# Kernel optimization log

Measured on AMD Instinct MI355X. Metric: run time of the kernel, lower is better.

The kernel has to match this reference:

```python
import jax, jax.numpy as jnp
import numpy as np

B, S, D, F, E, K, H = 4, 1024, 512, 2048, 8, 2, 8
HEAD_DIM = D // H


def setup_inputs() -> dict:
    key = jax.random.key(0)
    ks = jax.random.split(key, 8)
    s = 0.02
    return {
        "x": jax.random.normal(ks[0], (B, S, D), jnp.float32),
        "gate_Wk": jax.random.normal(ks[1], (D, D), jnp.float32) * s,
        "gate_bk": jnp.zeros((D,), jnp.float32),
        "expert_queries": jax.random.normal(ks[2], (E, D), jnp.float32),
        "Wqkv": jax.random.normal(ks[3], (E, 3 * D, D), jnp.float32) * s,
        "bqkv": jnp.zeros((E, 3 * D), jnp.float32),
        "Wo": jax.random.normal(ks[4], (E, D, D), jnp.float32) * s,
        "bo": jnp.zeros((E, D), jnp.float32),
        "g1": jnp.ones((E, D), jnp.float32),
        "be1": jnp.zeros((E, D), jnp.float32),
        "W1": jax.random.normal(ks[5], (E, F, D), jnp.float32) * s,
        "bf1": jnp.zeros((E, F), jnp.float32),
        "W2": jax.random.normal(ks[6], (E, D, F), jnp.float32) * s,
        "bf2": jnp.zeros((E, D), jnp.float32),
        "g2": jnp.ones((E, D), jnp.float32),
        "be2": jnp.zeros((E, D), jnp.float32),
    }


def _layernorm(x, g, b):
    m = x.mean(-1, keepdims=True)
    v = ((x - m) ** 2).mean(-1, keepdims=True)
    return (x - m) * jax.lax.rsqrt(v + 1e-5) * g + b


def _expert(x, Wqkv, bqkv, Wo, bo, g1, be1, W1, bf1, W2, bf2, g2, be2):
    # x: [B,S,D]; one ExpertTransformerDecoder block (dropout=0, eval)
    b, s, d = x.shape
    qkv = x @ Wqkv.T + bqkv                      # [B,S,3D]
    q, k, v = jnp.split(qkv, 3, axis=-1)
    to_heads = lambda t: t.reshape(b, s, H, HEAD_DIM).transpose(0, 2, 1, 3)
    q, k, v = to_heads(q), to_heads(k), to_heads(v)
    scale = 1.0 / np.sqrt(HEAD_DIM).astype(np.float32)
    attn = jax.nn.softmax(jnp.einsum('bhqd,bhkd->bhqk', q * scale, k), axis=-1)
    ctx = jnp.einsum('bhqk,bhkd->bhqd', attn, v).transpose(0, 2, 1, 3).reshape(b, s, d)
    ctx = ctx @ Wo.T + bo
    x = _layernorm(x + ctx, g1, be1)
    h = jax.nn.gelu(x @ W1.T + bf1, approximate=False)
    h = jax.nn.gelu(h @ W2.T + bf2, approximate=False)
    return _layernorm(x + h, g2, be2)


def reference(x, gate_Wk, gate_bk, expert_queries, Wqkv, bqkv, Wo, bo,
              g1, be1, W1, bf1, W2, bf2, g2, be2):
    # attention gating: softmax over experts of <key_proj(x), expert_q> * d^-0.5
    keys = x @ gate_Wk.T + gate_bk                      # [B,S,D]
    scores = jnp.einsum('bsd,ed->bse', keys, expert_queries) * (D ** -0.5)
    probs = jax.nn.softmax(scores, axis=-1)             # [B,S,E]
    # top-k mask + renormalize
    _, idx = jax.lax.top_k(probs, K)                    # [B,S,K]
    mask = jax.nn.one_hot(idx, E, dtype=probs.dtype).sum(-2)
    gated = probs * mask
    gated = gated / (gated.sum(-1, keepdims=True) + 1e-9)
    # run all experts densely (as the torch code does), vmapped over E
    eo = jax.vmap(_expert, in_axes=(None,) + (0,) * 12)(
        x, Wqkv, bqkv, Wo, bo, g1, be1, W1, bf1, W2, bf2, g2, be2)  # [E,B,S,D]
    return jnp.einsum('ebsd,bse->bsd', eo, gated)
```

## Files before the change

### kernel.cpp

```cpp
#include <hip/hip_runtime.h>
#include <cstdint>
#include <cmath>

#define Bc 4
#define Sc 1024
#define Dc 512
#define Fc 2048
#define Ec 8
#define Hc 8
#define Mc 4096

typedef unsigned short u16;
typedef __attribute__((ext_vector_type(8))) short bf16x8;
typedef __attribute__((ext_vector_type(4))) float f32x4;

__device__ __forceinline__ float bf2f(u16 u) {
  unsigned v = ((unsigned)u) << 16;
  return __builtin_bit_cast(float, v);
}
__device__ __forceinline__ u16 f2bf(float f) {
  unsigned u = __builtin_bit_cast(unsigned, f);
  unsigned r = 0x7fffu + ((u >> 16) & 1u);
  return (u16)((u + r) >> 16);
}
__device__ __forceinline__ unsigned pack2bf(float a, float b) {
  return (unsigned)f2bf(a) | ((unsigned)f2bf(b) << 16);
}
__device__ __forceinline__ float gelu_f(float x) {
  const float z = 1.5957691216057308f * fmaf(0.044715f * x, x * x, x);
  const float e = __expf(z);
  return x * (1.0f - __builtin_amdgcn_rcpf(e + 1.0f));
}
__device__ __forceinline__ void async16(const void* g, void* l) {
  __builtin_amdgcn_global_load_lds(
      (const __attribute__((address_space(1))) unsigned int*)g,
      (__attribute__((address_space(3))) unsigned int*)l, 16, 0, 0);
}

__global__ __launch_bounds__(256) void cvt_kernel(const float* __restrict__ in,
                                                  u16* __restrict__ outp, long long n) {
  const long long i = ((long long)blockIdx.x * 256 + threadIdx.x) * 4;
  if (i < n) {
    const float4 v = *(const float4*)(in + i);
    ushort4 o;
    o.x = f2bf(v.x); o.y = f2bf(v.y); o.z = f2bf(v.z); o.w = f2bf(v.w);
    *(ushort4*)(outp + i) = o;
  }
}

__global__ __launch_bounds__(256) void weq_kernel(const float* __restrict__ gWk,
                                                  const float* __restrict__ eq,
                                                  float* __restrict__ weq) {
  __shared__ float red[4][64];
  const int tid = threadIdx.x, wave = tid >> 6, lane = tid & 63;
  const int d = blockIdx.x * 64 + lane;
  const int e = blockIdx.y;
  float acc = 0.f;
  for (int j = wave * 128; j < wave * 128 + 128; ++j)
    acc += gWk[(long long)j * 512 + d] * eq[e * 512 + j];
  red[wave][lane] = acc;
  __syncthreads();
  if (wave == 0)
    weq[e * 512 + d] = red[0][lane] + red[1][lane] + red[2][lane] + red[3][lane];
}
__global__ void beq_kernel(const float* __restrict__ gbk, const float* __restrict__ eq,
                           float* __restrict__ beq) {
  const int wave = threadIdx.x >> 6, lane = threadIdx.x & 63;
  for (int e = wave; e < 8; e += 4) {
    float a = 0.f;
#pragma unroll
    for (int i = 0; i < 8; ++i) a += gbk[lane + 64 * i] * eq[e * 512 + lane + 64 * i];
#pragma unroll
    for (int off = 32; off; off >>= 1) a += __shfl_xor(a, off);
    if (lane == 0) beq[e] = a;
  }
}

__global__ __launch_bounds__(256) void gate_kernel(const float* __restrict__ x,
                                                   const float* __restrict__ weq,
                                                   const float* __restrict__ beq,
                                                   float* __restrict__ gated,
                                                   int* __restrict__ cnt, int* __restrict__ tlist,
                                                   int* __restrict__ pos) {
  const int wave = threadIdx.x >> 6, lane = threadIdx.x & 63;
  const int t = blockIdx.x * 4 + wave;
  const float* xr = x + (long long)t * 512;
  float acc[8] = {};
#pragma unroll
  for (int i = 0; i < 8; ++i) {
    const float xv = xr[lane + 64 * i];
#pragma unroll
    for (int e2 = 0; e2 < 8; ++e2) acc[e2] += xv * weq[e2 * 512 + lane + 64 * i];
  }
#pragma unroll
  for (int e2 = 0; e2 < 8; ++e2)
#pragma unroll
    for (int off = 32; off; off >>= 1) acc[e2] += __shfl_xor(acc[e2], off);
  if (lane == 0) {
    const float scale = 0.044194173824159216f;
    float s[8], mx = -1e30f;
#pragma unroll
    for (int e2 = 0; e2 < 8; ++e2) { s[e2] = (acc[e2] + beq[e2]) * scale; mx = fmaxf(mx, s[e2]); }
    float p[8], sum = 0.f;
#pragma unroll
    for (int e2 = 0; e2 < 8; ++e2) { p[e2] = expf(s[e2] - mx); sum += p[e2]; }
#pragma unroll
    for (int e2 = 0; e2 < 8; ++e2) p[e2] /= sum;
    int i1 = 0;
#pragma unroll
    for (int e2 = 1; e2 < 8; ++e2) if (p[e2] > p[i1]) i1 = e2;
    int i2 = (i1 == 0) ? 1 : 0;
#pragma unroll
    for (int e2 = 0; e2 < 8; ++e2) if (e2 != i1 && e2 != i2 && p[e2] > p[i2]) i2 = e2;
    const float denom = p[i1] + p[i2] + 1e-9f;
#pragma unroll
    for (int e2 = 0; e2 < 8; ++e2)
      gated[t * 8 + e2] = (e2 == i1 || e2 == i2) ? p[e2] / denom : 0.f;
    const int b = t >> 10;
    int s1 = atomicAdd(cnt + i1 * 4 + b, 1);
    tlist[(i1 * 4 + b) * 1024 + s1] = t;
    pos[i1 * 4096 + t] = s1;
    int s2 = atomicAdd(cnt + i2 * 4 + b, 1);
    tlist[(i2 * 4 + b) * 1024 + s2] = t;
    pos[i2 * 4096 + t] = s2;
  }
}

__global__ void pad_kernel(const int* __restrict__ cnt, int* __restrict__ tlist) {
  const int seg = blockIdx.x;
  const int c = cnt[seg];
  const int ce = (c + 127) & ~127;
  const int tpad = (seg & 3) << 10;
  for (int i = c + (int)threadIdx.x; i < ce; i += 128) tlist[seg * 1024 + i] = tpad;
}

__global__ void wl_kernel(const int* __restrict__ cnt, int* __restrict__ wl) {
  const int seg = threadIdx.x;
  if (seg >= 32) return;
  int base = 0;
  for (int s = 0; s < seg; ++s) base += (cnt[s] + 127) >> 7;
  const int nt = (cnt[seg] + 127) >> 7;
  for (int t = 0; t < nt; ++t) wl[base + t] = (seg << 8) | t;
  if (seg == 31) wl[96] = base + nt;
}

template <int GELU, int QKV, int ROUTED, int BK>
__global__ __launch_bounds__(256) void gemm_bf16(
    const u16* __restrict__ A, const u16* __restrict__ Bw, const float* __restrict__ bias,
    u16* __restrict__ Cout, u16* __restrict__ vT, int M, int N, int K, long long Astride,
    const int* __restrict__ wl) {
  int e;
  long long bm;
  if (ROUTED) {
    const int total = wl[96];
    if ((int)blockIdx.x >= total) return;
    const int item = wl[blockIdx.x];
    const int seg = item >> 8, tile = item & 255;
    e = seg >> 2;
    bm = ((long long)(seg & 3) << 10) + tile * 128;
  } else {
    e = blockIdx.z;
    bm = (long long)blockIdx.x * 128;
  }
  __shared__ __attribute__((aligned(16))) u16 As[128 * BK];
  __shared__ __attribute__((aligned(16))) u16 Bs[128 * BK];
  const int tid = threadIdx.x;
  const int wave = tid >> 6, lane = tid & 63;
  const long long bn = (long long)blockIdx.y * 128;
  const u16* Ag = A + (long long)e * Astride + bm * K;
  const u16* Bg = Bw + ((long long)e * N + bn) * K;
  constexpr int LPR = BK / 8;
  constexpr int RPI = 512 / BK;
  constexpr int IPW = BK / 16;
  const int lrow = lane / LPR, lpos = lane % LPR;
  const int lm = lane & 15, quad = lane >> 4;
  const int wm = (wave >> 1) * 64, wn = (wave & 1) * 64;
  f32x4 acc[4][4] = {};
  for (int kk = 0; kk < K; kk += BK) {
    __syncthreads();
#pragma unroll
    for (int i = 0; i < IPW; ++i) {
      const int gi = wave * IPW + i;
      const int row = gi * RPI + lrow;
      const int sc = lpos ^ (row & 7);
      async16(Ag + (long long)row * K + kk + sc * 8, &As[gi * 512]);
      async16(Bg + (long long)row * K + kk + sc * 8, &Bs[gi * 512]);
    }
    __syncthreads();
#pragma unroll
    for (int ks = 0; ks < BK / 32; ++ks) {
      bf16x8 af[4], bfr[4];
#pragma unroll
      for (int mi = 0; mi < 4; ++mi) {
        const int row = wm + mi * 16 + lm;
        const int ch = (ks * 4 + quad) ^ (row & 7);
        af[mi] = *(const bf16x8*)(As + row * BK + ch * 8);
      }
#pragma unroll
      for (int nj = 0; nj < 4; ++nj) {
        const int row = wn + nj * 16 + lm;
        const int ch = (ks * 4 + quad) ^ (row & 7);
        bfr[nj] = *(const bf16x8*)(Bs + row * BK + ch * 8);
      }
#pragma unroll
      for (int mi = 0; mi < 4; ++mi)
#pragma unroll
        for (int nj = 0; nj < 4; ++nj)
          acc[mi][nj] = __builtin_amdgcn_mfma_f32_16x16x32_bf16(bfr[nj], af[mi], acc[mi][nj], 0, 0, 0);
    }
  }
  const float* bs = bias + (long long)e * N;
#pragma unroll
  for (int mi = 0; mi < 4; ++mi) {
    const int m = (int)bm + wm + mi * 16 + lm;
#pragma unroll
    for (int nj = 0; nj < 4; ++nj) {
      const int n0 = (int)bn + wn + nj * 16 + quad * 4;
      const float4 bv = *(const float4*)(bs + n0);
      float v0 = acc[mi][nj][0] + bv.x;
      float v1 = acc[mi][nj][1] + bv.y;
      float v2 = acc[mi][nj][2] + bv.z;
      float v3 = acc[mi][nj][3] + bv.w;
      if (GELU) { v0 = gelu_f(v0); v1 = gelu_f(v1); v2 = gelu_f(v2); v3 = gelu_f(v3); }
      if (QKV) {
        if (n0 < 1024) {
          uint2 pk; pk.x = pack2bf(v0, v1); pk.y = pack2bf(v2, v3);
          *(uint2*)(Cout + ((long long)e * Mc + m) * 1024 + n0) = pk;
        } else {
          const int hh = (n0 - 1024) >> 6, dd = (n0 - 1024) & 63;
          const int bb = m >> 10, ss = m & 1023;
          u16* vp = vT + ((((long long)e * Bc + bb) * Hc + hh) * 64 + dd) * Sc + ss;
          vp[0] = f2bf(v0); vp[Sc] = f2bf(v1); vp[2 * Sc] = f2bf(v2); vp[3 * Sc] = f2bf(v3);
        }
      } else {
        uint2 pk; pk.x = pack2bf(v0, v1); pk.y = pack2bf(v2, v3);
        *(uint2*)(Cout + ((long long)e * M + m) * N + n0) = pk;
      }
    }
  }
}

__global__ __launch_bounds__(256, 1) void attn_fused(const u16* __restrict__ qk,
                                                     const u16* __restrict__ vT,
                                                     u16* __restrict__ ctx,
                                                     const int* __restrict__ cnt,
                                                     const int* __restrict__ tlist) {
  const int bh = blockIdx.x;
  const int b = bh >> 3, h = bh & 7;
  const int e = blockIdx.y;
  const int seg = (e << 2) + b;
  const int ce = (cnt[seg] + 127) & ~127;
  const int T = ce >> 6;
  if (T == 0) return;
  __shared__ __attribute__((aligned(16))) u16 Ks[64 * 64];
  __shared__ __attribute__((aligned(16))) u16 Vs[64 * 64];
  __shared__ __attribute__((aligned(16))) u16 Pl[4][16 * 72];
  const int tid = threadIdx.x, wave = tid >> 6, lane = tid & 63;
  const int lm = lane & 15, quad = lane >> 4;
  const u16* qkbase = qk + (long long)e * Mc * 1024;
  const u16* vbase = vT + ((((long long)e * Bc + b) * Hc + h) * 64) * Sc;
  const int lr = lane >> 3, lc = (lane & 7) ^ lr;
  u16* P = &Pl[wave][0];
  unsigned* P32 = (unsigned*)P;
  const int pwbase = lm * 36 + quad * 2;

  for (int qg = 0; qg < T; qg += 4) {
    const int tcnt = (T - qg < 4) ? (T - qg) : 4;
    bf16x8 aq[4][2];
    f32x4 O[4][4] = {};
    float lsum[4] = {0.f, 0.f, 0.f, 0.f};
#pragma unroll
    for (int t = 0; t < 4; ++t)
      if (t < tcnt) {
        const int pidx = seg * 1024 + (qg + t) * 64 + wave * 16 + lm;
        const int tq = tlist[pidx];
#pragma unroll
        for (int ks = 0; ks < 2; ++ks)
          aq[t][ks] = *(const bf16x8*)(qkbase + (long long)tq * 1024 + h * 64 + ks * 32 + quad * 8);
      }
    for (int n0 = 0; n0 < Sc; n0 += 64) {
      __syncthreads();
#pragma unroll
      for (int i = 0; i < 2; ++i) {
        const int rg = wave * 2 + i;
        const int row = rg * 8 + lr;
        async16(qkbase + ((long long)b * Sc + n0 + row) * 1024 + 512 + h * 64 + lc * 8,
                &Ks[rg * 512]);
        async16(vbase + (long long)row * Sc + n0 + lc * 8, &Vs[rg * 512]);
      }
      __syncthreads();
      bf16x8 kf[4][2];
#pragma unroll
      for (int kj = 0; kj < 4; ++kj) {
        const int row = kj * 16 + lm;
        kf[kj][0] = *(const bf16x8*)(Ks + row * 64 + ((quad) ^ (row & 7)) * 8);
        kf[kj][1] = *(const bf16x8*)(Ks + row * 64 + ((4 + quad) ^ (row & 7)) * 8);
      }
      bf16x8 ap[4][2];
#pragma unroll
      for (int t = 0; t < 4; ++t)
        if (t < tcnt) {
          f32x4 sT[4];
#pragma unroll
          for (int kj = 0; kj < 4; ++kj) {
            f32x4 c = {};
            c = __builtin_amdgcn_mfma_f32_16x16x32_bf16(kf[kj][0], aq[t][0], c, 0, 0, 0);
            c = __builtin_amdgcn_mfma_f32_16x16x32_bf16(kf[kj][1], aq[t][1], c, 0, 0, 0);
            sT[kj] = c;
          }
#pragma unroll
          for (int kj = 0; kj < 4; ++kj) {
            const float p0 = __expf(sT[kj][0] * 0.125f);
            const float p1 = __expf(sT[kj][1] * 0.125f);
            const float p2 = __expf(sT[kj][2] * 0.125f);
            const float p3 = __expf(sT[kj][3] * 0.125f);
            lsum[t] += (p0 + p1) + (p2 + p3);
            P32[pwbase + kj * 8 + 0] = pack2bf(p0, p1);
            P32[pwbase + kj * 8 + 1] = pack2bf(p2, p3);
          }
          asm volatile("s_waitcnt lgkmcnt(0)" ::: "memory");
          ap[t][0] = *(const bf16x8*)(P + lm * 72 + quad * 8);
          ap[t][1] = *(const bf16x8*)(P + lm * 72 + 32 + quad * 8);
        }
#pragma unroll
      for (int d4 = 0; d4 < 4; ++d4) {
        const int row = d4 * 16 + lm;
        bf16x8 v0 = *(const bf16x8*)(Vs + row * 64 + ((quad) ^ (row & 7)) * 8);
        bf16x8 v1 = *(const bf16x8*)(Vs + row * 64 + ((4 + quad) ^ (row & 7)) * 8);
#pragma unroll
        for (int t = 0; t < 4; ++t)
          if (t < tcnt) {
            O[t][d4] = __builtin_amdgcn_mfma_f32_16x16x32_bf16(v0, ap[t][0], O[t][d4], 0, 0, 0);
            O[t][d4] = __builtin_amdgcn_mfma_f32_16x16x32_bf16(v1, ap[t][1], O[t][d4], 0, 0, 0);
          }
      }
    }
#pragma unroll
    for (int t = 0; t < 4; ++t)
      if (t < tcnt) {
        float ls = lsum[t];
        ls += __shfl_xor(ls, 16);
        ls += __shfl_xor(ls, 32);
        const float inv = 1.0f / ls;
        const long long pidx = seg * 1024 + (qg + t) * 64 + wave * 16 + lm;
#pragma unroll
        for (int d4 = 0; d4 < 4; ++d4) {
          uint2 pk;
          pk.x = pack2bf(O[t][d4][0] * inv, O[t][d4][1] * inv);
          pk.y = pack2bf(O[t][d4][2] * inv, O[t][d4][3] * inv);
          *(uint2*)(ctx + pidx * 512 + h * 64 + d4 * 16 + quad * 4) = pk;
        }
      }
  }
}

__global__ __launch_bounds__(256) void ln1_kernel(const float* __restrict__ x,
                                                  const u16* __restrict__ ctxp,
                                                  const float* __restrict__ g1,
                                                  const float* __restrict__ be1,
                                                  u16* __restrict__ x1,
                                                  const int* __restrict__ cnt,
                                                  const int* __restrict__ tlist) {
  const int i = blockIdx.x, b = blockIdx.y, e = blockIdx.z;
  const int seg = (e << 2) + b;
  const int ce = (cnt[seg] + 127) & ~127;
  if (i >= ce) return;
  const long long p = seg * 1024 + i;
  const int t = tlist[p];
  const int tid = threadIdx.x;
  const int wave = tid >> 6, lane = tid & 63;
  __shared__ float sred[4], qred[4];
  const float v0 = x[(long long)t * 512 + tid] + bf2f(ctxp[p * 512 + tid]);
  const float v1 = x[(long long)t * 512 + tid + 256] + bf2f(ctxp[p * 512 + tid + 256]);
  float s = v0 + v1, q = v0 * v0 + v1 * v1;
#pragma unroll
  for (int off = 32; off; off >>= 1) { s += __shfl_xor(s, off); q += __shfl_xor(q, off); }
  if (lane == 0) { sred[wave] = s; qred[wave] = q; }
  __syncthreads();
  s = sred[0] + sred[1] + sred[2] + sred[3];
  q = qred[0] + qred[1] + qred[2] + qred[3];
  const float mean = s * (1.0f / 512.0f);
  const float var = q * (1.0f / 512.0f) - mean * mean;
  const float rstd = rsqrtf(var + 1e-5f);
  x1[p * 512 + tid] = f2bf((v0 - mean) * rstd * g1[e * 512 + tid] + be1[e * 512 + tid]);
  x1[p * 512 + tid + 256] =
      f2bf((v1 - mean) * rstd * g1[e * 512 + tid + 256] + be1[e * 512 + tid + 256]);
}

__global__ __launch_bounds__(256) void ln2_kernel(const u16* __restrict__ x1,
                                                  const u16* __restrict__ h2,
                                                  const float* __restrict__ g2,
                                                  const float* __restrict__ be2,
                                                  const float* __restrict__ gated,
                                                  const int* __restrict__ pos,
                                                  float* __restrict__ out) {
  const int t = blockIdx.x, tid = threadIdx.x;
  const int b = t >> 10;
  const int wave = tid >> 6, lane = tid & 63;
  __shared__ float sred[4], qred[4];
  float o0 = 0.f, o1 = 0.f;
  for (int e = 0; e < 8; ++e) {
    const float wgt = gated[t * 8 + e];
    if (wgt != 0.f) {
      const long long p = ((e << 2) + b) * 1024 + pos[e * 4096 + t];
      const float v0 = bf2f(x1[p * 512 + tid]) + bf2f(h2[p * 512 + tid]);
      const float v1 = bf2f(x1[p * 512 + tid + 256]) + bf2f(h2[p * 512 + tid + 256]);
      float s = v0 + v1, q = v0 * v0 + v1 * v1;
#pragma unroll
      for (int off = 32; off; off >>= 1) { s += __shfl_xor(s, off); q += __shfl_xor(q, off); }
      if (lane == 0) { sred[wave] = s; qred[wave] = q; }
      __syncthreads();
      s = sred[0] + sred[1] + sred[2] + sred[3];
      q = qred[0] + qred[1] + qred[2] + qred[3];
      __syncthreads();
      const float mean = s * (1.0f / 512.0f);
      const float var = q * (1.0f / 512.0f) - mean * mean;
      const float rstd = rsqrtf(var + 1e-5f);
      o0 += wgt * ((v0 - mean) * rstd * g2[e * 512 + tid] + be2[e * 512 + tid]);
      o1 += wgt * ((v1 - mean) * rstd * g2[e * 512 + tid + 256] + be2[e * 512 + tid + 256]);
    }
  }
  out[(long long)t * 512 + tid] = o0;
  out[(long long)t * 512 + tid + 256] = o1;
}

extern "C" void kernel_launch(void* const* d_in, const int* in_sizes, int n_in, void* d_out,
                              int out_size, void* d_ws, size_t ws_size, hipStream_t stream) {
  const float* x    = (const float*)d_in[0];
  const float* gWk  = (const float*)d_in[1];
  const float* gbk  = (const float*)d_in[2];
  const float* eq   = (const float*)d_in[3];
  const float* Wqkv = (const float*)d_in[4];
  const float* bqkv = (const float*)d_in[5];
  const float* Wo   = (const float*)d_in[6];
  const float* bo   = (const float*)d_in[7];
  const float* g1   = (const float*)d_in[8];
  const float* be1  = (const float*)d_in[9];
  const float* W1   = (const float*)d_in[10];
  const float* bf1  = (const float*)d_in[11];
  const float* W2   = (const float*)d_in[12];
  const float* bf2  = (const float*)d_in[13];
  const float* g2   = (const float*)d_in[14];
  const float* be2  = (const float*)d_in[15];
  float* out = (float*)d_out;

  char* wsp = (char*)d_ws;
  size_t off = 0;
  auto take = [&](size_t bytes) -> void* {
    void* p = wsp + off;
    off += (bytes + 255) & ~(size_t)255;
    return p;
  };
  u16* xb    = (u16*)take((size_t)Mc * 512 * 2);
  u16* Wqkvb = (u16*)take((size_t)Ec * 1536 * 512 * 2);
  u16* Wob   = (u16*)take((size_t)Ec * 512 * 512 * 2);
  u16* W1b   = (u16*)take((size_t)Ec * 2048 * 512 * 2);
  u16* W2b   = (u16*)take((size_t)Ec * 512 * 2048 * 2);
  float* weq   = (float*)take(8 * 512 * 4);
  float* beqb  = (float*)take(8 * 4);
  float* gated = (float*)take((size_t)Mc * 8 * 4);
  int* cnt   = (int*)take(32 * 4);
  int* tlist = (int*)take(32 * 1024 * 4);
  int* pos   = (int*)take((size_t)Ec * Mc * 4);
  int* wl    = (int*)take(128 * 4);
  char* big = (char*)take(134217728);
  u16* qkb  = (u16*)big;
  u16* vTb  = (u16*)(big + 67108864);
  u16* ctxp = (u16*)(big + 100663296);
  u16* hb   = (u16*)big;
  u16* ctxb = (u16*)take(33554432);
  u16* h2b  = ctxb;
  u16* x1b  = (u16*)take(33554432);
  (void)in_sizes; (void)n_in; (void)out_size; (void)ws_size;

  cvt_kernel<<<dim3(2048), dim3(256), 0, stream>>>(x, xb, (long long)Mc * 512);
  cvt_kernel<<<dim3(6144), dim3(256), 0, stream>>>(Wqkv, Wqkvb, (long long)Ec * 1536 * 512);
  cvt_kernel<<<dim3(2048), dim3(256), 0, stream>>>(Wo, Wob, (long long)Ec * 512 * 512);
  cvt_kernel<<<dim3(8192), dim3(256), 0, stream>>>(W1, W1b, (long long)Ec * 2048 * 512);
  cvt_kernel<<<dim3(8192), dim3(256), 0, stream>>>(W2, W2b, (long long)Ec * 512 * 2048);
  hipMemsetAsync(cnt, 0, 32 * 4, stream);
  weq_kernel<<<dim3(8, 8), dim3(256), 0, stream>>>(gWk, eq, weq);
  beq_kernel<<<dim3(1), dim3(256), 0, stream>>>(gbk, eq, beqb);
  gate_kernel<<<dim3(1024), dim3(256), 0, stream>>>(x, weq, beqb, gated, cnt, tlist, pos);
  pad_kernel<<<dim3(32), dim3(128), 0, stream>>>(cnt, tlist);
  wl_kernel<<<dim3(1), dim3(64), 0, stream>>>(cnt, wl);
  gemm_bf16<0, 1, 0, 64><<<dim3(32, 12, 8), dim3(256), 0, stream>>>(xb, Wqkvb, bqkv, qkb, vTb, Mc, 1536, 512, 0LL, wl);
  attn_fused<<<dim3(32, 8), dim3(256), 0, stream>>>(qkb, vTb, ctxb, cnt, tlist);
  gemm_bf16<0, 0, 1, 128><<<dim3(96, 4), dim3(256), 0, stream>>>(ctxb, Wob, bo, ctxp, nullptr, Mc, 512, 512, (long long)Mc * 512, wl);
  ln1_kernel<<<dim3(1024, 4, 8), dim3(256), 0, stream>>>(x, ctxp, g1, be1, x1b, cnt, tlist);
  gemm_bf16<1, 0, 1, 128><<<dim3(96, 16), dim3(256), 0, stream>>>(x1b, W1b, bf1, hb, nullptr, Mc, 2048, 512, (long long)Mc * 512, wl);
  gemm_bf16<1, 0, 1, 128><<<dim3(96, 4), dim3(256), 0, stream>>>(hb, W2b, bf2, h2b, nullptr, Mc, 512, 2048, (long long)Mc * 2048, wl);
  ln2_kernel<<<dim3(4096), dim3(256), 0, stream>>>(x1b, h2b, g2, be2, gated, pos, out);
}
```

Measured before the change: 526.6 us.

## Split routed attention into per-64-query-tile blocks via work list

New measurement: 509.7 us. 1.03x faster.

```diff
diff --git a/kernel.cpp b/kernel.cpp
--- a/kernel.cpp
+++ b/kernel.cpp
@@ -141,7 +141,8 @@
   for (int s = 0; s < seg; ++s) base += (cnt[s] + 127) >> 7;
   const int nt = (cnt[seg] + 127) >> 7;
   for (int t = 0; t < nt; ++t) wl[base + t] = (seg << 8) | t;
-  if (seg == 31) wl[96] = base + nt;
+  for (int t = 0; t < 2 * nt; ++t) wl[128 + 2 * base + t] = (seg << 8) | t;
+  if (seg == 31) { wl[96] = base + nt; wl[97] = 2 * (base + nt); }
 }
 
 template <int GELU, int QKV, int ROUTED, int BK>
@@ -240,18 +241,15 @@
   }
 }
 
-__global__ __launch_bounds__(256, 1) void attn_fused(const u16* __restrict__ qk,
-                                                     const u16* __restrict__ vT,
-                                                     u16* __restrict__ ctx,
-                                                     const int* __restrict__ cnt,
-                                                     const int* __restrict__ tlist) {
-  const int bh = blockIdx.x;
-  const int b = bh >> 3, h = bh & 7;
-  const int e = blockIdx.y;
-  const int seg = (e << 2) + b;
-  const int ce = (cnt[seg] + 127) & ~127;
-  const int T = ce >> 6;
-  if (T == 0) return;
+__global__ __launch_bounds__(256, 4) void attn_tile(const u16* __restrict__ qk,
+                                                    const u16* __restrict__ vT,
+                                                    u16* __restrict__ ctx,
+                                                    const int* __restrict__ wl,
+                                                    const int* __restrict__ tlist) {
+  if ((int)blockIdx.x >= wl[97]) return;
+  const int item = wl[128 + blockIdx.x];
+  const int seg = item >> 8, qt = item & 255;
+  const int e = seg >> 2, b = seg & 3, h = blockIdx.y;
   __shared__ __attribute__((aligned(16))) u16 Ks[64 * 64];
   __shared__ __attribute__((aligned(16))) u16 Vs[64 * 64];
   __shared__ __attribute__((aligned(16))) u16 Pl[4][16 * 72];
@@ -264,93 +262,69 @@
   unsigned* P32 = (unsigned*)P;
   const int pwbase = lm * 36 + quad * 2;
 
-  for (int qg = 0; qg < T; qg += 4) {
-    const int tcnt = (T - qg < 4) ? (T - qg) : 4;
-    bf16x8 aq[4][2];
-    f32x4 O[4][4] = {};
-    float lsum[4] = {0.f, 0.f, 0.f, 0.f};
-#pragma unroll
-    for (int t = 0; t < 4; ++t)
-      if (t < tcnt) {
-        const int pidx = seg * 1024 + (qg + t) * 64 + wave * 16 + lm;
-        const int tq = tlist[pidx];
-#pragma unroll
-        for (int ks = 0; ks < 2; ++ks)
-          aq[t][ks] = *(const bf16x8*)(qkbase + (long long)tq * 1024 + h * 64 + ks * 32 + quad * 8);
-      }
-    for (int n0 = 0; n0 < Sc; n0 += 64) {
-      __syncthreads();
-#pragma unroll
-      for (int i = 0; i < 2; ++i) {
-        const int rg = wave * 2 + i;
-        const int row = rg * 8 + lr;
-        async16(qkbase + ((long long)b * Sc + n0 + row) * 1024 + 512 + h * 64 + lc * 8,
-                &Ks[rg * 512]);
-        async16(vbase + (long long)row * Sc + n0 + lc * 8, &Vs[rg * 512]);
-      }
-      __syncthreads();
-      bf16x8 kf[4][2];
-#pragma unroll
-      for (int kj = 0; kj < 4; ++kj) {
-        const int row = kj * 16 + lm;
-        kf[kj][0] = *(const bf16x8*)(Ks + row * 64 + ((quad) ^ (row & 7)) * 8);
-        kf[kj][1] = *(const bf16x8*)(Ks + row * 64 + ((4 + quad) ^ (row & 7)) * 8);
-      }
-      bf16x8 ap[4][2];
-#pragma unroll
-      for (int t = 0; t < 4; ++t)
-        if (t < tcnt) {
-          f32x4 sT[4];
-#pragma unroll
-          for (int kj = 0; kj < 4; ++kj) {
-            f32x4 c = {};
-            c = __builtin_amdgcn_mfma_f32_16x16x32_bf16(kf[kj][0], aq[t][0], c, 0, 0, 0);
-            c = __builtin_amdgcn_mfma_f32_16x16x32_bf16(kf[kj][1], aq[t][1], c, 0, 0, 0);
-            sT[kj] = c;
-          }
-#pragma unroll
-          for (int kj = 0; kj < 4; ++kj) {
-            const float p0 = __expf(sT[kj][0] * 0.125f);
-            const float p1 = __expf(sT[kj][1] * 0.125f);
-            const float p2 = __expf(sT[kj][2] * 0.125f);
-            const float p3 = __expf(sT[kj][3] * 0.125f);
-            lsum[t] += (p0 + p1) + (p2 + p3);
-            P32[pwbase + kj * 8 + 0] = pack2bf(p0, p1);
-            P32[pwbase + kj * 8 + 1] = pack2bf(p2, p3);
-          }
-          asm volatile("s_waitcnt lgkmcnt(0)" ::: "memory");
-          ap[t][0] = *(const bf16x8*)(P + lm * 72 + quad * 8);
-          ap[t][1] = *(const bf16x8*)(P + lm * 72 + 32 + quad * 8);
-        }
-#pragma unroll
-      for (int d4 = 0; d4 < 4; ++d4) {
-        const int row = d4 * 16 + lm;
-        bf16x8 v0 = *(const bf16x8*)(Vs + row * 64 + ((quad) ^ (row & 7)) * 8);
-        bf16x8 v1 = *(const bf16x8*)(Vs + row * 64 + ((4 + quad) ^ (row & 7)) * 8);
-#pragma unroll
-        for (int t = 0; t < 4; ++t)
-          if (t < tcnt) {
-            O[t][d4] = __builtin_amdgcn_mfma_f32_16x16x32_bf16(v0, ap[t][0], O[t][d4], 0, 0, 0);
-            O[t][d4] = __builtin_amdgcn_mfma_f32_16x16x32_bf16(v1, ap[t][1], O[t][d4], 0, 0, 0);
-          }
-      }
-    }
-#pragma unroll
-    for (int t = 0; t < 4; ++t)
-      if (t < tcnt) {
-        float ls = lsum[t];
-        ls += __shfl_xor(ls, 16);
-        ls += __shfl_xor(ls, 32);
-        const float inv = 1.0f / ls;
-        const long long pidx = seg * 1024 + (qg + t) * 64 + wave * 16 + lm;
-#pragma unroll
-        for (int d4 = 0; d4 < 4; ++d4) {
-          uint2 pk;
-          pk.x = pack2bf(O[t][d4][0] * inv, O[t][d4][1] * inv);
-          pk.y = pack2bf(O[t][d4][2] * inv, O[t][d4][3] * inv);
-          *(uint2*)(ctx + pidx * 512 + h * 64 + d4 * 16 + quad * 4) = pk;
-        }
-      }
+  const long long pidx = (long long)seg * 1024 + qt * 64 + wave * 16 + lm;
+  const int tq = tlist[pidx];
+  bf16x8 aq[2];
+#pragma unroll
+  for (int ks = 0; ks < 2; ++ks)
+    aq[ks] = *(const bf16x8*)(qkbase + (long long)tq * 1024 + h * 64 + ks * 32 + quad * 8);
+  f32x4 O[4] = {};
+  float lsum = 0.f;
+
+  for (int n0 = 0; n0 < Sc; n0 += 64) {
+    __syncthreads();
+#pragma unroll
+    for (int i = 0; i < 2; ++i) {
+      const int rg = wave * 2 + i;
+      const int row = rg * 8 + lr;
+      async16(qkbase + ((long long)b * Sc + n0 + row) * 1024 + 512 + h * 64 + lc * 8,
+              &Ks[rg * 512]);
+      async16(vbase + (long long)row * Sc + n0 + lc * 8, &Vs[rg * 512]);
+    }
+    __syncthreads();
+    f32x4 sT[4];
+#pragma unroll
+    for (int kj = 0; kj < 4; ++kj) {
+      const int row = kj * 16 + lm;
+      const bf16x8 k0 = *(const bf16x8*)(Ks + row * 64 + ((quad) ^ (row & 7)) * 8);
+      const bf16x8 k1 = *(const bf16x8*)(Ks + row * 64 + ((4 + quad) ^ (row & 7)) * 8);
+      f32x4 c = {};
+      c = __builtin_amdgcn_mfma_f32_16x16x32_bf16(k0, aq[0], c, 0, 0, 0);
+      c = __builtin_amdgcn_mfma_f32_16x16x32_bf16(k1, aq[1], c, 0, 0, 0);
+      sT[kj] = c;
+    }
+#pragma unroll
+    for (int kj = 0; kj < 4; ++kj) {
+      const float p0 = __expf(sT[kj][0] * 0.125f);
+      const float p1 = __expf(sT[kj][1] * 0.125f);
+      const float p2 = __expf(sT[kj][2] * 0.125f);
+      const float p3 = __expf(sT[kj][3] * 0.125f);
+      lsum += (p0 + p1) + (p2 + p3);
+      P32[pwbase + kj * 8 + 0] = pack2bf(p0, p1);
+      P32[pwbase + kj * 8 + 1] = pack2bf(p2, p3);
+    }
+    asm volatile("s_waitcnt lgkmcnt(0)" ::: "memory");
+    const bf16x8 ap0 = *(const bf16x8*)(P + lm * 72 + quad * 8);
+    const bf16x8 ap1 = *(const bf16x8*)(P + lm * 72 + 32 + quad * 8);
+#pragma unroll
+    for (int d4 = 0; d4 < 4; ++d4) {
+      const int row = d4 * 16 + lm;
+      const bf16x8 v0 = *(const bf16x8*)(Vs + row * 64 + ((quad) ^ (row & 7)) * 8);
+      const bf16x8 v1 = *(const bf16x8*)(Vs + row * 64 + ((4 + quad) ^ (row & 7)) * 8);
+      O[d4] = __builtin_amdgcn_mfma_f32_16x16x32_bf16(v0, ap0, O[d4], 0, 0, 0);
+      O[d4] = __builtin_amdgcn_mfma_f32_16x16x32_bf16(v1, ap1, O[d4], 0, 0, 0);
+    }
+  }
+  float ls = lsum;
+  ls += __shfl_xor(ls, 16);
+  ls += __shfl_xor(ls, 32);
+  const float inv = 1.0f / ls;
+#pragma unroll
+  for (int d4 = 0; d4 < 4; ++d4) {
+    uint2 pk;
+    pk.x = pack2bf(O[d4][0] * inv, O[d4][1] * inv);
+    pk.y = pack2bf(O[d4][2] * inv, O[d4][3] * inv);
+    *(uint2*)(ctx + pidx * 512 + h * 64 + d4 * 16 + quad * 4) = pk;
   }
 }
 
@@ -462,7 +436,7 @@
   int* cnt   = (int*)take(32 * 4);
   int* tlist = (int*)take(32 * 1024 * 4);
   int* pos   = (int*)take((size_t)Ec * Mc * 4);
-  int* wl    = (int*)take(128 * 4);
+  int* wl    = (int*)take(512 * 4);
   char* big = (char*)take(134217728);
   u16* qkb  = (u16*)big;
   u16* vTb  = (u16*)(big + 67108864);
@@ -485,7 +459,7 @@
   pad_kernel<<<dim3(32), dim3(128), 0, stream>>>(cnt, tlist);
   wl_kernel<<<dim3(1), dim3(64), 0, stream>>>(cnt, wl);
   gemm_bf16<0, 1, 0, 64><<<dim3(32, 12, 8), dim3(256), 0, stream>>>(xb, Wqkvb, bqkv, qkb, vTb, Mc, 1536, 512, 0LL, wl);
-  attn_fused<<<dim3(32, 8), dim3(256), 0, stream>>>(qkb, vTb, ctxb, cnt, tlist);
+  attn_tile<<<dim3(192, 8), dim3(256), 0, stream>>>(qkb, vTb, ctxb, wl, tlist);
   gemm_bf16<0, 0, 1, 128><<<dim3(96, 4), dim3(256), 0, stream>>>(ctxb, Wob, bo, ctxp, nullptr, Mc, 512, 512, (long long)Mc * 512, wl);
   ln1_kernel<<<dim3(1024, 4, 8), dim3(256), 0, stream>>>(x, ctxp, g1, be1, x1b, cnt, tlist);
   gemm_bf16<1, 0, 1, 128><<<dim3(96, 16), dim3(256), 0, stream>>>(x1b, W1b, bf1, hb, nullptr, Mc, 2048, 512, (long long)Mc * 512, wl);
```
